# Kernel tuning notes

Measured on AMD Instinct MI355X. Metric: run time of the kernel, lower is better.

Reference implementation:

```python
import jax, jax.numpy as jnp
import numpy as np

RES = 64          # img_resolution
SIGMA = 1.0       # Gaussian kernel sigma
PI = RES * RES    # flattened persistence image size
B, P0, P1 = 256, 1024, 512
EPS_P = 1e-6
EPS_D = 1e-8
LN_EPS = 1e-5


def setup_inputs() -> dict:
    key = jax.random.key(0)
    ks = jax.random.split(key, 8)
    pairs_h0 = jax.random.uniform(ks[0], (B, P0, 2), dtype=jnp.float32)
    pairs_h1 = jax.random.uniform(ks[1], (B, P1, 2), dtype=jnp.float32)
    W1 = jax.random.normal(ks[2], (2 * PI, 512), dtype=jnp.float32) * 0.02
    W2 = jax.random.normal(ks[3], (512, 256), dtype=jnp.float32) * 0.02
    W3 = jax.random.normal(ks[4], (256, 128), dtype=jnp.float32) * 0.02
    return dict(
        pairs_h0=pairs_h0, pairs_h1=pairs_h1,
        W1=W1, b1=jnp.zeros((512,), jnp.float32), g1=jnp.ones((512,), jnp.float32), be1=jnp.zeros((512,), jnp.float32),
        W2=W2, b2=jnp.zeros((256,), jnp.float32), g2=jnp.ones((256,), jnp.float32), be2=jnp.zeros((256,), jnp.float32),
        W3=W3, b3=jnp.zeros((128,), jnp.float32),
    )


def _masked_minmax(x, valid):
    big = jnp.float32(1e30)
    mn = jnp.min(jnp.where(valid, x, big))
    mx = jnp.max(jnp.where(valid, x, -big))
    degen = (mx - mn) < 1e-6
    mn = jnp.where(degen, 0.0, mn)
    mx = jnp.where(degen, 1.0, mx)
    return mn, mx


def _pers_image(pairs):
    """pairs: [P, 2] (birth, death) -> [RES, RES] persistence image."""
    births = pairs[:, 0]
    pers = pairs[:, 1] - pairs[:, 0]
    valid = pers > EPS_P
    any_valid = jnp.any(valid)
    bmin, bmax = _masked_minmax(births, valid)
    pmin, pmax = _masked_minmax(pers, valid)
    bn = (births - bmin) / (bmax - bmin + EPS_D)   # [P]
    pn = (pers - pmin) / (pmax - pmin + EPS_D)     # [P]
    w = jnp.where(valid, pers, 0.0)                # weight = persistence, invalid -> 0
    grid = jnp.linspace(0.0, 1.0, RES)
    inv2s2 = 1.0 / (2.0 * SIGMA * SIGMA)
    kb = jnp.exp(-((grid[None, :] - bn[:, None]) ** 2) * inv2s2)  # [P, RES] over b_grid
    kp = jnp.exp(-((grid[None, :] - pn[:, None]) ** 2) * inv2s2)  # [P, RES] over p_grid
    # img[i, j] = sum_p w_p * exp(-(bdiff_p[i] + pdiff_p[j]) / 2s^2)  (separable Gaussian)
    img = jnp.einsum('p,pi,pj->ij', w, kb, kp)
    return jnp.where(any_valid, img, jnp.zeros_like(img))


def _layernorm(x, g, b):
    mu = jnp.mean(x, axis=-1, keepdims=True)
    var = jnp.mean((x - mu) ** 2, axis=-1, keepdims=True)
    return (x - mu) * jax.lax.rsqrt(var + LN_EPS) * g + b


def reference(pairs_h0, pairs_h1, W1, b1, g1, be1, W2, b2, g2, be2, W3, b3):
    bsz = pairs_h0.shape[0]
    pi0 = jax.vmap(_pers_image)(pairs_h0).reshape(bsz, -1)  # [B, RES*RES]
    pi1 = jax.vmap(_pers_image)(pairs_h1).reshape(bsz, -1)
    feats = jnp.concatenate([pi0, pi1], axis=1)             # [B, 2*PI]
    h = jax.nn.relu(_layernorm(feats @ W1 + b1, g1, be1))   # dropout: eval mode (identity)
    h = jax.nn.relu(_layernorm(h @ W2 + b2, g2, be2))
    return h @ W3 + b3
```

## Files before the change

kernel.cpp:

```cpp
#include <hip/hip_runtime.h>
#include <hip/hip_bf16.h>
#include <hip/hip_fp16.h>


#define P0_N 1024
#define P1_N 512

typedef _Float16 h2 __attribute__((ext_vector_type(2)));
typedef _Float16 f16x8 __attribute__((ext_vector_type(8)));
typedef float f32x4 __attribute__((ext_vector_type(4)));

#define KSCALE 0.849321804f
#define DG (KSCALE / 63.0f)

static __device__ __forceinline__ float fast_exp2(float x) {
#if defined(__has_builtin)
#if __has_builtin(__builtin_amdgcn_exp2f)
    return __builtin_amdgcn_exp2f(x);
#else
    return exp2f(x);
#endif
#else
    return exp2f(x);
#endif
}

static __device__ __forceinline__ h2 pk2(float a, float b) {
#if defined(__has_builtin)
#if __has_builtin(__builtin_amdgcn_cvt_pkrtz)
    return __builtin_bit_cast(h2, __builtin_amdgcn_cvt_pkrtz(a, b));
#else
    h2 r; r[0] = (_Float16)a; r[1] = (_Float16)b; return r;
#endif
#else
    h2 r; r[0] = (_Float16)a; r[1] = (_Float16)b; return r;
#endif
}

__global__ __launch_bounds__(256) void pi_kernel(const float* __restrict__ p0,
                                                 const float* __restrict__ p1,
                                                 _Float16* __restrict__ featsH)
{
    const int task = blockIdx.x;
    const int b    = task >> 1;
    const int hom  = task & 1;
    const int P    = hom ? P1_N : P0_N;
    const float* pairs = hom ? (p1 + (size_t)b * P1_N * 2)
                             : (p0 + (size_t)b * P0_N * 2);
    const int t = threadIdx.x;
    const int w = t >> 6, lane = t & 63;

    __shared__ float cbs[1024], cps[1024], cws[1024];
    __shared__ __align__(16) _Float16 kbT[2][64][72];
    __shared__ __align__(16) _Float16 kpT[2][64][72];
    __shared__ float wmn0[4], wmx0[4], wmn1[4], wmx1[4];
    __shared__ unsigned gcnt[16];

    float bv_[4], pv_[4];
    bool  val[4];
    float bmin = 1e30f, bmax = -1e30f, pmin = 1e30f, pmax = -1e30f;
    #pragma unroll
    for (int s = 0; s < 4; ++s) {
        const int p = t + s * 256;
        val[s] = false; bv_[s] = 0.0f; pv_[s] = 0.0f;
        if (p < P) {
            const float2 pr = ((const float2*)pairs)[p];
            const float birth = pr.x;
            const float pers  = pr.y - pr.x;
            bv_[s] = birth; pv_[s] = pers;
            val[s] = pers > 1e-6f;
            if (val[s]) {
                bmin = fminf(bmin, birth); bmax = fmaxf(bmax, birth);
                pmin = fminf(pmin, pers);  pmax = fmaxf(pmax, pers);
            }
        }
    }
    #pragma unroll
    for (int d = 32; d > 0; d >>= 1) {
        bmin = fminf(bmin, __shfl_xor(bmin, d));
        bmax = fmaxf(bmax, __shfl_xor(bmax, d));
        pmin = fminf(pmin, __shfl_xor(pmin, d));
        pmax = fmaxf(pmax, __shfl_xor(pmax, d));
    }
    unsigned long long msk[4];
    #pragma unroll
    for (int s = 0; s < 4; ++s) msk[s] = __ballot(val[s]);
    if (lane == 0) {
        wmn0[w] = bmin; wmx0[w] = bmax; wmn1[w] = pmin; wmx1[w] = pmax;
        #pragma unroll
        for (int s = 0; s < 4; ++s) gcnt[w * 4 + s] = (unsigned)__popcll(msk[s]);
    }
    __syncthreads();
    float bmn = fminf(fminf(wmn0[0], wmn0[1]), fminf(wmn0[2], wmn0[3]));
    float bmx = fmaxf(fmaxf(wmx0[0], wmx0[1]), fmaxf(wmx0[2], wmx0[3]));
    float pmn = fminf(fminf(wmn1[0], wmn1[1]), fminf(wmn1[2], wmn1[3]));
    float pmx = fmaxf(fmaxf(wmx1[0], wmx1[1]), fmaxf(wmx1[2], wmx1[3]));
    if (bmx - bmn < 1e-6f) { bmn = 0.0f; bmx = 1.0f; }
    if (pmx - pmn < 1e-6f) { pmn = 0.0f; pmx = 1.0f; }
    const float binv = KSCALE / (bmx - bmn + 1e-8f);
    const float pinv = KSCALE / (pmx - pmn + 1e-8f);

    unsigned gb[4] = {0, 0, 0, 0};
    unsigned run = 0;
    #pragma unroll
    for (int g = 0; g < 16; ++g) {
        #pragma unroll
        for (int s = 0; s < 4; ++s)
            if (g == w * 4 + s) gb[s] = run;
        run += gcnt[g];
    }
    const int nv = (int)run;
    const int nchunks = (nv + 63) >> 6;

    const unsigned long long below = (1ull << lane) - 1ull;
    #pragma unroll
    for (int s = 0; s < 4; ++s) {
        if (val[s]) {
            const unsigned pos = gb[s] + (unsigned)__popcll(msk[s] & below);
            cbs[pos] = (bv_[s] - bmn) * binv;
            cps[pos] = (pv_[s] - pmn) * pinv;
            cws[pos] = pv_[s];
        }
    }
    for (int i = nv + t; i < nchunks * 64; i += 256) {
        cbs[i] = 0.0f; cps[i] = 0.0f; cws[i] = 0.0f;
    }

    const int pp   = lane & 31;
    const int surf = lane >> 5;
    const int c0   = w * 16;
    const float Gq  = (float)c0 * DG;
    const float rho = fast_exp2(-2.0f * DG * DG);
    const float c1  = -DG * DG * (float)(2 * c0 + 1);
    const float* Xarr = surf ? cps : cbs;

    const int wm = (w >> 1) * 32, wn = (w & 1) * 32;
    const int fr = lane & 15, fg = lane >> 4;

    f32x4 acc[2][2] = {};

    auto gen_chunk = [&](int c, int bi) {
        const int base = c * 64;
        const float X0 = Xarr[base + 2 * pp];
        const float X1 = Xarr[base + 2 * pp + 1];
        float W0 = 1.0f, W1 = 1.0f;
        if (!surf) { W0 = cws[base + 2 * pp]; W1 = cws[base + 2 * pp + 1]; }
        const float d0 = Gq - X0, d1 = Gq - X1;
        float v0 = W0 * fast_exp2(-(d0 * d0));
        float v1 = W1 * fast_exp2(-(d1 * d1));
        float r0 = fast_exp2(c1 + 2.0f * DG * X0);
        float r1 = fast_exp2(c1 + 2.0f * DG * X1);
        _Float16* sT = surf ? &kpT[bi][0][0] : &kbT[bi][0][0];
        #pragma unroll
        for (int j = 0; j < 16; ++j) {
            *(h2*)&sT[(c0 + j) * 72 + 2 * pp] = pk2(v0, v1);
            v0 *= r0; r0 *= rho;
            v1 *= r1; r1 *= rho;
        }
    };
    auto consume_chunk = [&](int bi) {
        #pragma unroll
        for (int ks2 = 0; ks2 < 64; ks2 += 32) {
            f16x8 af[2], bf[2];
            af[0] = *(const f16x8*)&kbT[bi][wm + fr][ks2 + fg * 8];
            af[1] = *(const f16x8*)&kbT[bi][wm + 16 + fr][ks2 + fg * 8];
            bf[0] = *(const f16x8*)&kpT[bi][wn + fr][ks2 + fg * 8];
            bf[1] = *(const f16x8*)&kpT[bi][wn + 16 + fr][ks2 + fg * 8];
            #pragma unroll
            for (int i = 0; i < 2; ++i)
                #pragma unroll
                for (int j = 0; j < 2; ++j)
                    acc[i][j] = __builtin_amdgcn_mfma_f32_16x16x32_f16(
                        af[i], bf[j], acc[i][j], 0, 0, 0);
        }
    };

    __syncthreads();
    if (nchunks > 0) gen_chunk(0, 0);
    __syncthreads();
    for (int c = 0; c < nchunks; ++c) {
        if (c + 1 < nchunks) gen_chunk(c + 1, (c + 1) & 1);
        consume_chunk(c & 1);
        __syncthreads();
    }

    _Float16* dst = featsH + (size_t)b * 8192 + hom * 4096;
    #pragma unroll
    for (int i = 0; i < 2; ++i)
        #pragma unroll
        for (int j = 0; j < 2; ++j) {
            const int r0_ = wm + i * 16 + fg * 4;
            const int cc  = wn + j * 16 + fr;
            #pragma unroll
            for (int r = 0; r < 4; ++r)
                dst[(size_t)(r0_ + r) * 64 + cc] = (_Float16)acc[i][j][r];
        }
}

__global__ __launch_bounds__(256) void gemm1_mfma(const _Float16* __restrict__ Ah,
                                                  const float* __restrict__ W1,
                                                  float* __restrict__ part)
{
    const int mt = blockIdx.x;
    const int nt = blockIdx.y;
    const int ks = blockIdx.z;
    const int t  = threadIdx.x;

    __shared__ _Float16 As[64][72];
    __shared__ _Float16 Bs[64][72];

    const int mbase = mt * 64, nbase = nt * 64, kbase = ks * 256;
    const int lrow = t >> 2, lk0 = (t & 3) * 16;
    const int k0s  = (t >> 4) * 4, nc = (t & 15) * 4;

    const _Float16* Ap = Ah + (size_t)(mbase + lrow) * 8192 + kbase + lk0;
    const float*    Wp = W1 + (size_t)(kbase + k0s) * 512 + nbase + nc;

    const int w = t >> 6, lane = t & 63;
    const int wm = (w >> 1) * 32, wn = (w & 1) * 32;
    const int fr = lane & 15, fg = lane >> 4;

    f32x4 acc[2][2] = {};

    uint4  pa0 = *(const uint4*)(Ap);
    uint4  pa1 = *(const uint4*)(Ap + 8);
    float4 pw0 = *(const float4*)(Wp);
    float4 pw1 = *(const float4*)(Wp + 512);
    float4 pw2 = *(const float4*)(Wp + 1024);
    float4 pw3 = *(const float4*)(Wp + 1536);

    for (int k0 = 0; k0 < 256; k0 += 64) {
        __syncthreads();
        *(uint4*)&As[lrow][lk0]     = pa0;
        *(uint4*)&As[lrow][lk0 + 8] = pa1;
        {
            union { uint2 u; h2 h[2]; } pk;
            pk.h[0] = pk2(pw0.x, pw1.x); pk.h[1] = pk2(pw2.x, pw3.x);
            *(uint2*)&Bs[nc + 0][k0s] = pk.u;
            pk.h[0] = pk2(pw0.y, pw1.y); pk.h[1] = pk2(pw2.y, pw3.y);
            *(uint2*)&Bs[nc + 1][k0s] = pk.u;
            pk.h[0] = pk2(pw0.z, pw1.z); pk.h[1] = pk2(pw2.z, pw3.z);
            *(uint2*)&Bs[nc + 2][k0s] = pk.u;
            pk.h[0] = pk2(pw0.w, pw1.w); pk.h[1] = pk2(pw2.w, pw3.w);
            *(uint2*)&Bs[nc + 3][k0s] = pk.u;
        }
        __syncthreads();
        if (k0 + 64 < 256) {
            pa0 = *(const uint4*)(Ap + k0 + 64);
            pa1 = *(const uint4*)(Ap + k0 + 72);
            const float* wn_ = Wp + (size_t)(k0 + 64) * 512;
            pw0 = *(const float4*)(wn_);
            pw1 = *(const float4*)(wn_ + 512);
            pw2 = *(const float4*)(wn_ + 1024);
            pw3 = *(const float4*)(wn_ + 1536);
        }
        #pragma unroll
        for (int ks2 = 0; ks2 < 64; ks2 += 32) {
            f16x8 af[2], bf[2];
            af[0] = *(const f16x8*)&As[wm + fr][ks2 + fg * 8];
            af[1] = *(const f16x8*)&As[wm + 16 + fr][ks2 + fg * 8];
            bf[0] = *(const f16x8*)&Bs[wn + fr][ks2 + fg * 8];
            bf[1] = *(const f16x8*)&Bs[wn + 16 + fr][ks2 + fg * 8];
            #pragma unroll
            for (int i = 0; i < 2; ++i)
                #pragma unroll
                for (int j = 0; j < 2; ++j)
                    acc[i][j] = __builtin_amdgcn_mfma_f32_16x16x32_f16(
                        af[i], bf[j], acc[i][j], 0, 0, 0);
        }
    }

    #pragma unroll
    for (int i = 0; i < 2; ++i)
        #pragma unroll
        for (int j = 0; j < 2; ++j) {
            const int r0 = mbase + wm + i * 16 + fg * 4;
            const int c  = nbase + wn + j * 16 + fr;
            float* dst = part + (size_t)ks * (256 * 512) + (size_t)r0 * 512 + c;
            #pragma unroll
            for (int r = 0; r < 4; ++r) dst[(size_t)r * 512] = acc[i][j][r];
        }
}

__global__ __launch_bounds__(1024) void tail_kernel(const float* __restrict__ part,
    const float* __restrict__ b1, const float* __restrict__ g1, const float* __restrict__ be1,
    const float* __restrict__ W2, const float* __restrict__ b2, const float* __restrict__ g2, const float* __restrict__ be2,
    const float* __restrict__ W3, const float* __restrict__ b3,
    float* __restrict__ out)
{
    const int row  = blockIdx.x;
    const int t    = threadIdx.x;
    const int wid  = t >> 6, lane = t & 63;

    __shared__ float h1s[512];
    __shared__ float h2s[256];
    __shared__ float red[1024];
    __shared__ __align__(16) float red4[1024][4];
    __shared__ float wredA[16], wredB[16];

    const int col = t & 511, sb16 = (t >> 9) * 16;
    float v = 0.0f;
    #pragma unroll
    for (int s = 0; s < 16; ++s)
        v += part[(size_t)(sb16 + s) * (256 * 512) + (size_t)row * 512 + col];
    red[t] = v;
    __syncthreads();
    float x = 0.0f;
    if (t < 512) x = red[t] + red[t + 512] + b1[col];

    float s1 = (t < 512) ? x : 0.0f;
    float s2 = (t < 512) ? x * x : 0.0f;
    #pragma unroll
    for (int d = 32; d > 0; d >>= 1) {
        s1 += __shfl_xor(s1, d);
        s2 += __shfl_xor(s2, d);
    }
    if (lane == 0) { wredA[wid] = s1; wredB[wid] = s2; }
    __syncthreads();
    float mu = 0.0f, m2 = 0.0f;
    #pragma unroll
    for (int i = 0; i < 16; ++i) { mu += wredA[i]; m2 += wredB[i]; }
    mu *= (1.0f / 512.0f);
    m2  = m2 * (1.0f / 512.0f) - mu * mu;
    const float rs = rsqrtf(m2 + 1e-5f);
    if (t < 512) h1s[col] = fmaxf((x - mu) * rs * g1[col] + be1[col], 0.0f);
    __syncthreads();

    const int cg2 = t & 63, ksl = t >> 6;
    {
        float4 a4 = make_float4(0.0f, 0.0f, 0.0f, 0.0f);
        const float* w2p = W2 + (size_t)(ksl * 32) * 256 + cg2 * 4;
        const float* h1p = h1s + ksl * 32;
        #pragma unroll 8
        for (int k = 0; k < 32; ++k) {
            const float4 wv = *(const float4*)(w2p + (size_t)k * 256);
            const float hv = h1p[k];
            a4.x += hv * wv.x; a4.y += hv * wv.y;
            a4.z += hv * wv.z; a4.w += hv * wv.w;
        }
        *(float4*)red4[t] = a4;
    }
    __syncthreads();
    float y = 0.0f;
    if (t < 256) {
        const float* r4f = (const float*)red4;
        const int base = (t >> 2) * 4 + (t & 3);
        #pragma unroll
        for (int s = 0; s < 16; ++s) y += r4f[s * 256 + base];
        y += b2[t];
    }

    s1 = (t < 256) ? y : 0.0f;
    s2 = (t < 256) ? y * y : 0.0f;
    #pragma unroll
    for (int d = 32; d > 0; d >>= 1) {
        s1 += __shfl_xor(s1, d);
        s2 += __shfl_xor(s2, d);
    }
    if (lane == 0) { wredA[wid] = s1; wredB[wid] = s2; }
    __syncthreads();
    mu = 0.0f; m2 = 0.0f;
    #pragma unroll
    for (int i = 0; i < 16; ++i) { mu += wredA[i]; m2 += wredB[i]; }
    mu *= (1.0f / 256.0f);
    m2  = m2 * (1.0f / 256.0f) - mu * mu;
    const float rs2 = rsqrtf(m2 + 1e-5f);
    if (t < 256) h2s[t] = fmaxf((y - mu) * rs2 * g2[t] + be2[t], 0.0f);
    __syncthreads();

    const int col3 = t & 127, ks3 = t >> 7;
    float o = 0.0f;
    #pragma unroll 8
    for (int k = 0; k < 32; ++k)
        o += h2s[ks3 * 32 + k] * W3[(size_t)(ks3 * 32 + k) * 128 + col3];
    red[t] = o;
    __syncthreads();
    if (t < 128) {
        float oo = 0.0f;
        #pragma unroll
        for (int s = 0; s < 8; ++s) oo += red[t + s * 128];
        out[(size_t)row * 128 + t] = oo + b3[t];
    }
}

extern "C" void kernel_launch(void* const* d_in, const int* in_sizes, int n_in,
                              void* d_out, int out_size, void* d_ws, size_t ws_size,
                              hipStream_t stream)
{
    const float* p0  = (const float*)d_in[0];
    const float* p1  = (const float*)d_in[1];
    const float* W1  = (const float*)d_in[2];
    const float* b1  = (const float*)d_in[3];
    const float* g1  = (const float*)d_in[4];
    const float* be1 = (const float*)d_in[5];
    const float* W2  = (const float*)d_in[6];
    const float* b2  = (const float*)d_in[7];
    const float* g2  = (const float*)d_in[8];
    const float* be2 = (const float*)d_in[9];
    const float* W3  = (const float*)d_in[10];
    const float* b3  = (const float*)d_in[11];
    float* out = (float*)d_out;

    _Float16* featsH = (_Float16*)d_ws;
    float*    part   = (float*)((char*)d_ws + (4u << 20));

    hipLaunchKernelGGL(pi_kernel,    dim3(512),      dim3(256),  0, stream, p0, p1, featsH);
    hipLaunchKernelGGL(gemm1_mfma,   dim3(4, 8, 32), dim3(256),  0, stream, featsH, W1, part);
    hipLaunchKernelGGL(tail_kernel,  dim3(256),      dim3(1024), 0, stream, part,
                       b1, g1, be1, W2, b2, g2, be2, W3, b3, out);
}
```

Baseline: 43.61 us.

## Single-buffer PI kernel generation with wider thread mapping; halve GEMM1 split-K

The persistence-image kernel drops the double-buffered gen/consume pipeline for a single shared buffer. All 256 threads now generate each 64-pair chunk, each handling 8 pairs by 4 grid rows and writing 16-byte packed stores. Separately, GEMM1 split-K goes from 32 to 16 slices of 512 K each, and the tail reduction sums 16 partials instead of 32. This cuts partial-sum traffic and gen work per thread, but loses gen/MFMA overlap and leaves fewer GEMM blocks.

```diff
diff --git a/kernel.cpp b/kernel.cpp
--- a/kernel.cpp
+++ b/kernel.cpp
@@ -51,8 +51,8 @@
     const int w = t >> 6, lane = t & 63;
 
     __shared__ float cbs[1024], cps[1024], cws[1024];
-    __shared__ __align__(16) _Float16 kbT[2][64][72];
-    __shared__ __align__(16) _Float16 kpT[2][64][72];
+    __shared__ __align__(16) _Float16 kbT[64][72];
+    __shared__ __align__(16) _Float16 kpT[64][72];
     __shared__ float wmn0[4], wmx0[4], wmn1[4], wmx1[4];
     __shared__ unsigned gcnt[16];
 
@@ -126,46 +126,54 @@
         cbs[i] = 0.0f; cps[i] = 0.0f; cws[i] = 0.0f;
     }
 
-    const int pp   = lane & 31;
-    const int surf = lane >> 5;
-    const int c0   = w * 16;
-    const float Gq  = (float)c0 * DG;
-    const float rho = fast_exp2(-2.0f * DG * DG);
-    const float c1  = -DG * DG * (float)(2 * c0 + 1);
+    const int surf = t >> 7;
+    const int rem  = t & 127;
+    const int po   = rem & 7;
+    const int cq   = rem >> 3;
+    const float G0   = (float)(cq * 4) * DG;
+    const float rho  = fast_exp2(-2.0f * DG * DG);
+    const float c1q  = -DG * DG * (float)(8 * cq + 1);
     const float* Xarr = surf ? cps : cbs;
+    _Float16* sT = surf ? &kpT[0][0] : &kbT[0][0];
 
     const int wm = (w >> 1) * 32, wn = (w & 1) * 32;
     const int fr = lane & 15, fg = lane >> 4;
 
     f32x4 acc[2][2] = {};
 
-    auto gen_chunk = [&](int c, int bi) {
+    __syncthreads();
+    for (int c = 0; c < nchunks; ++c) {
         const int base = c * 64;
-        const float X0 = Xarr[base + 2 * pp];
-        const float X1 = Xarr[base + 2 * pp + 1];
-        float W0 = 1.0f, W1 = 1.0f;
-        if (!surf) { W0 = cws[base + 2 * pp]; W1 = cws[base + 2 * pp + 1]; }
-        const float d0 = Gq - X0, d1 = Gq - X1;
-        float v0 = W0 * fast_exp2(-(d0 * d0));
-        float v1 = W1 * fast_exp2(-(d1 * d1));
-        float r0 = fast_exp2(c1 + 2.0f * DG * X0);
-        float r1 = fast_exp2(c1 + 2.0f * DG * X1);
-        _Float16* sT = surf ? &kpT[bi][0][0] : &kbT[bi][0][0];
-        #pragma unroll
-        for (int j = 0; j < 16; ++j) {
-            *(h2*)&sT[(c0 + j) * 72 + 2 * pp] = pk2(v0, v1);
-            v0 *= r0; r0 *= rho;
-            v1 *= r1; r1 *= rho;
-        }
-    };
-    auto consume_chunk = [&](int bi) {
+        {
+            float v[8], r[8];
+            #pragma unroll
+            for (int p = 0; p < 8; ++p) {
+                const float X = Xarr[base + po * 8 + p];
+                const float W = surf ? 1.0f : cws[base + po * 8 + p];
+                const float d = G0 - X;
+                v[p] = W * fast_exp2(-(d * d));
+                r[p] = fast_exp2(c1q + 2.0f * DG * X);
+            }
+            #pragma unroll
+            for (int cc = 0; cc < 4; ++cc) {
+                union { uint4 u; h2 h[4]; } pk;
+                pk.h[0] = pk2(v[0], v[1]);
+                pk.h[1] = pk2(v[2], v[3]);
+                pk.h[2] = pk2(v[4], v[5]);
+                pk.h[3] = pk2(v[6], v[7]);
+                *(uint4*)&sT[(cq * 4 + cc) * 72 + po * 8] = pk.u;
+                #pragma unroll
+                for (int p = 0; p < 8; ++p) { v[p] *= r[p]; r[p] *= rho; }
+            }
+        }
+        __syncthreads();
         #pragma unroll
         for (int ks2 = 0; ks2 < 64; ks2 += 32) {
             f16x8 af[2], bf[2];
-            af[0] = *(const f16x8*)&kbT[bi][wm + fr][ks2 + fg * 8];
-            af[1] = *(const f16x8*)&kbT[bi][wm + 16 + fr][ks2 + fg * 8];
-            bf[0] = *(const f16x8*)&kpT[bi][wn + fr][ks2 + fg * 8];
-            bf[1] = *(const f16x8*)&kpT[bi][wn + 16 + fr][ks2 + fg * 8];
+            af[0] = *(const f16x8*)&kbT[wm + fr][ks2 + fg * 8];
+            af[1] = *(const f16x8*)&kbT[wm + 16 + fr][ks2 + fg * 8];
+            bf[0] = *(const f16x8*)&kpT[wn + fr][ks2 + fg * 8];
+            bf[1] = *(const f16x8*)&kpT[wn + 16 + fr][ks2 + fg * 8];
             #pragma unroll
             for (int i = 0; i < 2; ++i)
                 #pragma unroll
@@ -173,14 +181,6 @@
                     acc[i][j] = __builtin_amdgcn_mfma_f32_16x16x32_f16(
                         af[i], bf[j], acc[i][j], 0, 0, 0);
         }
-    };
-
-    __syncthreads();
-    if (nchunks > 0) gen_chunk(0, 0);
-    __syncthreads();
-    for (int c = 0; c < nchunks; ++c) {
-        if (c + 1 < nchunks) gen_chunk(c + 1, (c + 1) & 1);
-        consume_chunk(c & 1);
         __syncthreads();
     }
 
@@ -209,7 +209,7 @@
     __shared__ _Float16 As[64][72];
     __shared__ _Float16 Bs[64][72];
 
-    const int mbase = mt * 64, nbase = nt * 64, kbase = ks * 256;
+    const int mbase = mt * 64, nbase = nt * 64, kbase = ks * 512;
     const int lrow = t >> 2, lk0 = (t & 3) * 16;
     const int k0s  = (t >> 4) * 4, nc = (t & 15) * 4;
 
@@ -229,7 +229,7 @@
     float4 pw2 = *(const float4*)(Wp + 1024);
     float4 pw3 = *(const float4*)(Wp + 1536);
 
-    for (int k0 = 0; k0 < 256; k0 += 64) {
+    for (int k0 = 0; k0 < 512; k0 += 64) {
         __syncthreads();
         *(uint4*)&As[lrow][lk0]     = pa0;
         *(uint4*)&As[lrow][lk0 + 8] = pa1;
@@ -245,7 +245,7 @@
             *(uint2*)&Bs[nc + 3][k0s] = pk.u;
         }
         __syncthreads();
-        if (k0 + 64 < 256) {
+        if (k0 + 64 < 512) {
             pa0 = *(const uint4*)(Ap + k0 + 64);
             pa1 = *(const uint4*)(Ap + k0 + 72);
             const float* wn_ = Wp + (size_t)(k0 + 64) * 512;
@@ -298,11 +298,11 @@
     __shared__ __align__(16) float red4[1024][4];
     __shared__ float wredA[16], wredB[16];
 
-    const int col = t & 511, sb16 = (t >> 9) * 16;
+    const int col = t & 511, sb8 = (t >> 9) * 8;
     float v = 0.0f;
     #pragma unroll
-    for (int s = 0; s < 16; ++s)
-        v += part[(size_t)(sb16 + s) * (256 * 512) + (size_t)row * 512 + col];
+    for (int s = 0; s < 8; ++s)
+        v += part[(size_t)(sb8 + s) * (256 * 512) + (size_t)row * 512 + col];
     red[t] = v;
     __syncthreads();
     float x = 0.0f;
@@ -405,7 +405,7 @@
     float*    part   = (float*)((char*)d_ws + (4u << 20));
 
     hipLaunchKernelGGL(pi_kernel,    dim3(512),      dim3(256),  0, stream, p0, p1, featsH);
-    hipLaunchKernelGGL(gemm1_mfma,   dim3(4, 8, 32), dim3(256),  0, stream, featsH, W1, part);
+    hipLaunchKernelGGL(gemm1_mfma,   dim3(4, 8, 16), dim3(256),  0, stream, featsH, W1, part);
     hipLaunchKernelGGL(tail_kernel,  dim3(256),      dim3(1024), 0, stream, part,
                        b1, g1, be1, W2, b2, g2, be2, W3, b3, out);
 }
```

After: 42.20 us. -3.2%, faster.
